# Kernel tuning notes

Hardware: AMD Instinct MI355X
Metric: run time of the kernel (lower is better)

The kernel has to match this reference:

```python
import jax, jax.numpy as jnp
import numpy as np

TRNA_N, DIS_N = 8000, 6000
D, H, E, B = 128, 256, 320000, 16384
NEG_SLOPE = 0.2  # gat_alpha
TEMP = 0.5


def _gat(src, tgt, s_idx, t_idx, Wsrc, Wtgt, a, n_src):
    # BipartiteGraphAttentionLayer (eval mode, dropout off)
    h_i = src @ Wsrc.T            # [n_src, D]
    h_j = tgt @ Wtgt.T            # [n_tgt, D]
    # cat([h_i[s], h_j[t]]) @ a == (h_i @ a[:D])[s] + (h_j @ a[D:])[t]
    s_i = h_i @ a[:D]             # [n_src]
    s_j = h_j @ a[D:]             # [n_tgt]
    e = jax.nn.leaky_relu(s_i[s_idx] + s_j[t_idx], NEG_SLOPE)
    e = jnp.clip(e, -30.0, 30.0)
    exp_e = jnp.exp(e)
    denom = jax.ops.segment_sum(exp_e, s_idx, num_segments=n_src)
    alpha = exp_e / (denom[s_idx] + 1e-8)
    out = jax.ops.segment_sum(h_j[t_idx] * alpha[:, None], s_idx, num_segments=n_src)
    return jax.nn.elu(out)


def _hg(x, S):
    # HCCF-style parameter-free hypergraph conv: nodes -> hyperedges -> nodes
    return jax.nn.elu(S @ (S.T @ x))


def _info_nce(z1, z2):
    z1 = z1 / (jnp.linalg.norm(z1, axis=1, keepdims=True) + 1e-12)
    z2 = z2 / (jnp.linalg.norm(z2, axis=1, keepdims=True) + 1e-12)
    sim = (z1 @ z2.T) / TEMP      # [N, N]
    logp = jax.nn.log_softmax(sim, axis=1)
    return -jnp.mean(jnp.diagonal(logp))


def setup_inputs():
    key = jax.random.key(0)
    ks = jax.random.split(key, 20)
    xn = lambda k, shp, sc: jax.random.normal(k, shp, dtype=jnp.float32) * sc
    d2 = (2.0 / (2 * D)) ** 0.5
    return dict(
        trna_embed=xn(ks[0], (TRNA_N, D), (2.0 / (TRNA_N + D)) ** 0.5),
        disease_embed=xn(ks[1], (DIS_N, D), (2.0 / (DIS_N + D)) ** 0.5),
        thyper=xn(ks[2], (D, H), (2.0 / (D + H)) ** 0.5),
        dhyper=xn(ks[3], (D, H), (2.0 / (D + H)) ** 0.5),
        gat_t_Wsrc=xn(ks[4], (3, D, D), d2),
        gat_t_Wtgt=xn(ks[5], (3, D, D), d2),
        gat_t_a=xn(ks[6], (3, 2 * D), 1.414 * (2.0 / (2 * D + 1)) ** 0.5),
        gat_d_Wsrc=xn(ks[7], (3, D, D), d2),
        gat_d_Wtgt=xn(ks[8], (3, D, D), d2),
        gat_d_a=xn(ks[9], (3, 2 * D), 1.414 * (2.0 / (2 * D + 1)) ** 0.5),
        mlp_W1=xn(ks[10], (D, 2 * D), (2.0 / (3 * D)) ** 0.5),
        mlp_b1=jnp.zeros((D,), jnp.float32),
        mlp_W2=xn(ks[11], (1, D), (2.0 / (D + 1)) ** 0.5),
        mlp_b2=jnp.zeros((1,), jnp.float32),
        gate_W=xn(ks[12], (1, D), (2.0 / (D + 1)) ** 0.5),
        gate_b=jnp.zeros((1,), jnp.float32),
        src_id=jax.random.randint(ks[13], (E,), 0, TRNA_N),
        tgt_id=jax.random.randint(ks[14], (E,), 0, DIS_N),
        trna_ids=jax.random.randint(ks[15], (B,), 0, TRNA_N),
        disease_ids=jax.random.randint(ks[16], (B,), 0, DIS_N),
    )


def reference(trna_embed, disease_embed, thyper, dhyper,
              gat_t_Wsrc, gat_t_Wtgt, gat_t_a,
              gat_d_Wsrc, gat_d_Wtgt, gat_d_a,
              mlp_W1, mlp_b1, mlp_W2, mlp_b2, gate_W, gate_b,
              src_id, tgt_id, trna_ids, disease_ids):
    # stage 1: simple-graph GAT pass
    sg_t = _gat(trna_embed, disease_embed, src_id, tgt_id,
                gat_t_Wsrc[0], gat_t_Wtgt[0], gat_t_a[0], TRNA_N)
    sg_d = _gat(disease_embed, sg_t, tgt_id, src_id,
                gat_d_Wsrc[0], gat_d_Wtgt[0], gat_d_a[0], DIS_N)
    # hypergraph passes 1-2
    hg_t = _hg(sg_t, sg_t @ thyper)
    hg_d = _hg(sg_d, sg_d @ dhyper)
    hg_t = _hg(hg_t, hg_t @ thyper)
    hg_d = _hg(hg_d, hg_d @ dhyper)
    # GAT layers 2-3 on hypergraph outputs
    sg_t = _gat(hg_t, hg_d, src_id, tgt_id,
                gat_t_Wsrc[1], gat_t_Wtgt[1], gat_t_a[1], TRNA_N)
    sg_d = _gat(hg_d, hg_t, tgt_id, src_id,
                gat_d_Wsrc[1], gat_d_Wtgt[1], gat_d_a[1], DIS_N)
    sg_t = _gat(sg_t, sg_d, src_id, tgt_id,
                gat_t_Wsrc[2], gat_t_Wtgt[2], gat_t_a[2], TRNA_N)
    sg_d = _gat(sg_d, sg_t, tgt_id, src_id,
                gat_d_Wsrc[2], gat_d_Wtgt[2], gat_d_a[2], DIS_N)
    # hypergraph pass 3
    hg_t = _hg(hg_t, hg_t @ thyper)
    hg_d = _hg(hg_d, hg_d @ dhyper)
    final_t = sg_t + hg_t
    final_d = sg_d + hg_d
    sel_t = final_t[trna_ids]
    sel_d = final_d[disease_ids]
    contrast = _info_nce(sg_t, hg_t) + _info_nce(sg_d, hg_d)
    gmf_vec = sel_t * sel_d
    gmf_pred = jnp.sum(gmf_vec, axis=-1)
    mlp_in = jnp.concatenate([sel_t, sel_d], axis=-1)
    h1 = jax.nn.relu(mlp_in @ mlp_W1.T + mlp_b1)
    mlp_pred = (h1 @ mlp_W2.T + mlp_b2)[:, 0]
    gate = jax.nn.sigmoid(gmf_vec @ gate_W.T + gate_b)[:, 0]
    fusion_pred = gate * gmf_pred + (1.0 - gate) * mlp_pred
    return (fusion_pred, sg_t, sg_d, gmf_pred, mlp_pred, contrast)
```

## Files before the change

### kernel.cpp

```cpp
#include <hip/hip_runtime.h>
#include <math.h>

#define N_T 8000
#define N_D 6000
#define N_E 320000
#define N_B 16384
#define NSTRIP 24

typedef __attribute__((ext_vector_type(8))) short s16x8;
typedef __attribute__((ext_vector_type(8))) __bf16 bf16x8;
typedef __attribute__((ext_vector_type(4))) float f32x4;

static __device__ __forceinline__ f32x4 mfma16(s16x8 a, s16x8 b, f32x4 c) {
  return __builtin_amdgcn_mfma_f32_16x16x32_bf16(
      __builtin_bit_cast(bf16x8, a), __builtin_bit_cast(bf16x8, b), c, 0, 0, 0);
}

static __device__ __forceinline__ unsigned short f2bf(float f) {
  unsigned u = __float_as_uint(f);
  u += 0x7FFF + ((u >> 16) & 1);
  return (unsigned short)(u >> 16);
}

static __device__ __forceinline__ float bf2f(unsigned short u) {
  return __uint_as_float(((unsigned)u) << 16);
}

__device__ __forceinline__ float wave_sum(float v) {
  v += __shfl_xor(v, 32, 64);
  v += __shfl_xor(v, 16, 64);
  v += __shfl_xor(v, 8, 64);
  v += __shfl_xor(v, 4, 64);
  v += __shfl_xor(v, 2, 64);
  v += __shfl_xor(v, 1, 64);
  return v;
}

__global__ void k_hist2(const int* __restrict__ src, const int* __restrict__ tgt,
                        int* __restrict__ cnt) {
  int i = blockIdx.x * 256 + threadIdx.x;
  if (i < N_E) atomicAdd(&cnt[src[i]], 1);
  else if (i < 2 * N_E) atomicAdd(&cnt[N_T + tgt[i - N_E]], 1);
}

__global__ void k_scan2(const int* __restrict__ cnt, int* __restrict__ rp_t,
    int* __restrict__ cur_t, int* __restrict__ rp_d, int* __restrict__ cur_d) {
  const int* c = blockIdx.x ? cnt + N_T : cnt;
  const int n = blockIdx.x ? N_D : N_T;
  int* rp = blockIdx.x ? rp_d : rp_t;
  int* cur = blockIdx.x ? cur_d : cur_t;
  __shared__ int buf[1024];
  __shared__ int carry_s;
  if (threadIdx.x == 0) carry_s = 0;
  __syncthreads();
  for (int base = 0; base < n; base += 1024) {
    int c0 = carry_s;
    int i = base + (int)threadIdx.x;
    int v = (i < n) ? c[i] : 0;
    buf[threadIdx.x] = v;
    __syncthreads();
    for (int off = 1; off < 1024; off <<= 1) {
      int t = (threadIdx.x >= (unsigned)off) ? buf[threadIdx.x - off] : 0;
      __syncthreads();
      buf[threadIdx.x] += t;
      __syncthreads();
    }
    int incl = buf[threadIdx.x];
    if (i < n) { int e = c0 + incl - v; rp[i] = e; cur[i] = e; }
    __syncthreads();
    if (threadIdx.x == 0) carry_s = c0 + buf[1023];
    __syncthreads();
  }
  if (threadIdx.x == 0) rp[n] = carry_s;
}

__global__ void k_scatter2(const int* __restrict__ src, const int* __restrict__ tgt,
    int* __restrict__ cur_t, int* __restrict__ cur_d,
    int* __restrict__ nbr_t, int* __restrict__ nbr_d) {
  int i = blockIdx.x * 256 + threadIdx.x;
  if (i < N_E) {
    int p = atomicAdd(&cur_t[src[i]], 1);
    nbr_t[p] = tgt[i];
  } else if (i < 2 * N_E) {
    i -= N_E;
    int p = atomicAdd(&cur_d[tgt[i]], 1);
    nbr_d[p] = src[i];
  }
}

__global__ __launch_bounds__(256) void k_pgemm(const float* __restrict__ th,
    const float* __restrict__ dh, float* __restrict__ P_t, float* __restrict__ P_d) {
  const float* A = blockIdx.x < 4 ? th : dh;
  float* C = blockIdx.x < 4 ? P_t : P_d;
  const int sub = blockIdx.x & 3;
  const int row0 = (sub >> 1) * 64, col0 = (sub & 1) * 64;
  __shared__ float As[16][65];
  __shared__ float Bs[16][65];
  const int tid = threadIdx.x;
  const int tr = tid >> 4, tc = tid & 15;
  float acc[4][4] = {};
  for (int k0 = 0; k0 < 256; k0 += 16) {
    {
      int m = tid >> 2, kk = (tid & 3) * 4;
      float4 v = *(const float4*)(A + (size_t)(row0 + m) * 256 + k0 + kk);
      As[kk + 0][m] = v.x; As[kk + 1][m] = v.y; As[kk + 2][m] = v.z; As[kk + 3][m] = v.w;
    }
    {
      int nn = tid >> 2, kk = (tid & 3) * 4;
      float4 v = *(const float4*)(A + (size_t)(col0 + nn) * 256 + k0 + kk);
      Bs[kk + 0][nn] = v.x; Bs[kk + 1][nn] = v.y; Bs[kk + 2][nn] = v.z; Bs[kk + 3][nn] = v.w;
    }
    __syncthreads();
#pragma unroll
    for (int k = 0; k < 16; ++k) {
      float a[4], b[4];
#pragma unroll
      for (int i = 0; i < 4; ++i) a[i] = As[k][tr * 4 + i];
#pragma unroll
      for (int j = 0; j < 4; ++j) b[j] = Bs[k][tc * 4 + j];
#pragma unroll
      for (int i = 0; i < 4; ++i)
#pragma unroll
        for (int j = 0; j < 4; ++j)
          acc[i][j] = fmaf(a[i], b[j], acc[i][j]);
    }
    __syncthreads();
  }
#pragma unroll
  for (int i = 0; i < 4; ++i)
#pragma unroll
    for (int j = 0; j < 4; ++j)
      C[(size_t)(row0 + tr * 4 + i) * 128 + col0 + tc * 4 + j] = acc[i][j];
}

__global__ void k_tobf16m(const float* __restrict__ a0, unsigned short* __restrict__ y0,
    const float* __restrict__ a1, unsigned short* __restrict__ y1,
    const float* __restrict__ a2, unsigned short* __restrict__ y2,
    const float* __restrict__ a3, unsigned short* __restrict__ y3) {
  int i = blockIdx.x * 256 + threadIdx.x;
  const float* x; unsigned short* y;
  if (i < 12288) { x = a0; y = y0; }
  else if (i < 24576) { x = a1; y = y1; i -= 12288; }
  else if (i < 32768) { x = a2; y = y2; i -= 24576; }
  else if (i < 224768) { x = a3; y = y3; i -= 32768; }
  else return;
  float4 v = ((const float4*)x)[i];
  ushort4 o;
  o.x = f2bf(v.x); o.y = f2bf(v.y); o.z = f2bf(v.z); o.w = f2bf(v.w);
  ((ushort4*)y)[i] = o;
}

template<int K, int ACT, int BIAS, int SJMODE, int OUTF, int OUTB>
static __device__ __forceinline__ void mfma_body(
    const unsigned short* __restrict__ A, const unsigned short* __restrict__ B,
    const float* __restrict__ bias, const float* __restrict__ a2,
    float* __restrict__ Cf, unsigned short* __restrict__ Cb,
    float* __restrict__ sj_out, int M, int bx) {
  const int wave = threadIdx.x >> 6, lane = threadIdx.x & 63;
  const int row0 = bx * 32;
  const int col0 = wave * 32;
  const int l15 = lane & 15, kg = lane >> 4;
  constexpr int NS = K / 32;
  f32x4 acc[2][2] = {};
  s16x8 ab[2][2], bb[2][2];
  auto ld = [&](int buf, int k0) {
#pragma unroll
    for (int i = 0; i < 2; ++i) {
      int r = row0 + i * 16 + l15;
      ab[buf][i] = (r < M) ? *(const s16x8*)(A + (size_t)r * K + k0 + kg * 8) : (s16x8)0;
    }
#pragma unroll
    for (int j = 0; j < 2; ++j) {
      int c = col0 + j * 16 + l15;
      bb[buf][j] = *(const s16x8*)(B + (size_t)c * K + k0 + kg * 8);
    }
  };
  ld(0, 0);
#pragma unroll
  for (int s = 0; s < NS; ++s) {
    if (s + 1 < NS) ld((s + 1) & 1, (s + 1) * 32);
#pragma unroll
    for (int i = 0; i < 2; ++i)
#pragma unroll
      for (int j = 0; j < 2; ++j)
        acc[i][j] = mfma16(ab[s & 1][i], bb[s & 1][j], acc[i][j]);
  }
  __shared__ float sjl[4][32];
  float a2v[2];
  if (SJMODE) {
#pragma unroll
    for (int j = 0; j < 2; ++j) a2v[j] = a2[col0 + j * 16 + l15];
  }
#pragma unroll
  for (int i = 0; i < 2; ++i) {
    float part[4] = {0.f, 0.f, 0.f, 0.f};
#pragma unroll
    for (int j = 0; j < 2; ++j) {
      int gc = col0 + j * 16 + l15;
      float bv = BIAS ? bias[gc] : 0.f;
#pragma unroll
      for (int r = 0; r < 4; ++r) {
        int gr = row0 + i * 16 + kg * 4 + r;
        float v = acc[i][j][r] + bv;
        if (SJMODE == 1) part[r] += v * a2v[j];
        if (ACT == 1) v = v > 0.f ? v : __expf(v) - 1.f;
        if (ACT == 2) v = fmaxf(v, 0.f);
        if (SJMODE == 2) part[r] += v * a2v[j];
        if (gr < M) {
          if (OUTF) Cf[(size_t)gr * 128 + gc] = v;
          if (OUTB) Cb[(size_t)gr * 128 + gc] = f2bf(v);
        }
      }
    }
    if (SJMODE) {
#pragma unroll
      for (int r = 0; r < 4; ++r) {
        float p = part[r];
        p += __shfl_xor(p, 1, 64);
        p += __shfl_xor(p, 2, 64);
        p += __shfl_xor(p, 4, 64);
        p += __shfl_xor(p, 8, 64);
        if (l15 == 0) sjl[wave][i * 16 + kg * 4 + r] = p;
      }
    }
  }
  if (SJMODE) {
    __syncthreads();
    if (threadIdx.x < 32) {
      int gr = row0 + (int)threadIdx.x;
      if (gr < M)
        sj_out[gr] = sjl[0][threadIdx.x] + sjl[1][threadIdx.x] +
                     sjl[2][threadIdx.x] + sjl[3][threadIdx.x];
    }
  }
}

template<int K, int ACT, int BIAS, int SJMODE, int OUTF, int OUTB>
__global__ __launch_bounds__(256) void k_mfma(const unsigned short* __restrict__ A,
    const unsigned short* __restrict__ B, const float* __restrict__ bias,
    const float* __restrict__ a2, float* __restrict__ Cf, unsigned short* __restrict__ Cb,
    float* __restrict__ sj_out, int M) {
  mfma_body<K, ACT, BIAS, SJMODE, OUTF, OUTB>(A, B, bias, a2, Cf, Cb, sj_out, M, blockIdx.x);
}

template<int K, int ACT, int SJMODE, int OUTF, int OUTB>
__global__ __launch_bounds__(256) void k_mfma2(
    const unsigned short* __restrict__ A0, const unsigned short* __restrict__ B0,
    const float* __restrict__ a20, float* __restrict__ Cf0,
    unsigned short* __restrict__ Cb0, float* __restrict__ sj0, int M0, int G0,
    const unsigned short* __restrict__ A1, const unsigned short* __restrict__ B1,
    const float* __restrict__ a21, float* __restrict__ Cf1,
    unsigned short* __restrict__ Cb1, float* __restrict__ sj1, int M1) {
  int bx = blockIdx.x;
  if (bx < G0)
    mfma_body<K, ACT, 0, SJMODE, OUTF, OUTB>(A0, B0, nullptr, a20, Cf0, Cb0, sj0, M0, bx);
  else
    mfma_body<K, ACT, 0, SJMODE, OUTF, OUTB>(A1, B1, nullptr, a21, Cf1, Cb1, sj1, M1, bx - G0);
}

__global__ __launch_bounds__(256) void k_nce2m(
    const unsigned short* __restrict__ z1t, const unsigned short* __restrict__ z2t,
    float* __restrict__ rs_tp, float* __restrict__ dg_tp,
    const unsigned short* __restrict__ z1d, const unsigned short* __restrict__ z2d,
    float* __restrict__ rs_dp, float* __restrict__ dg_dp) {
  const int wave = threadIdx.x >> 6, lane = threadIdx.x & 63;
  const int l15 = lane & 15, kg = lane >> 4;
  int by = blockIdx.y;
  const unsigned short *z1, *z2; float *rowsum, *diagv; int M, N;
  if (by < 63) { z1 = z1t; z2 = z2t; rowsum = rs_tp; diagv = dg_tp; M = N_T; N = N_T; }
  else { by -= 63; z1 = z1d; z2 = z2d; rowsum = rs_dp; diagv = dg_dp; M = N_D; N = N_D; }
  const int row0 = by * 128 + (wave >> 1) * 64;
  const int CT = (N + 127) >> 7;
  const int ctps = (CT + NSTRIP - 1) / NSTRIP;
  const int ct0 = blockIdx.x * ctps;
  const int ct1 = min(CT, ct0 + ctps);
  if (ct0 >= CT) return;
  s16x8 a[4][4];
#pragma unroll
  for (int ks = 0; ks < 4; ++ks)
#pragma unroll
    for (int i = 0; i < 4; ++i) {
      int r = row0 + i * 16 + l15;
      a[ks][i] = (r < M) ? *(const s16x8*)(z1 + (size_t)r * 128 + ks * 32 + kg * 8) : (s16x8)0;
    }
  s16x8 b[2][4];
  auto ldb = [&](int buf, int ct, int ks) {
    int c0 = ct * 128 + (wave & 1) * 64;
#pragma unroll
    for (int j = 0; j < 4; ++j) {
      int c = c0 + j * 16 + l15;
      b[buf][j] = (c < N) ? *(const s16x8*)(z2 + (size_t)c * 128 + ks * 32 + kg * 8) : (s16x8)0;
    }
  };
  float rs[4][4] = {};
  ldb(0, ct0, 0);
  for (int ct = ct0; ct < ct1; ++ct) {
    const int col0 = ct * 128 + (wave & 1) * 64;
    f32x4 acc[4][4] = {};
#pragma unroll
    for (int ks = 0; ks < 4; ++ks) {
      if (ks < 3) ldb((ks + 1) & 1, ct, ks + 1);
      else if (ct + 1 < ct1) ldb(0, ct + 1, 0);
#pragma unroll
      for (int i = 0; i < 4; ++i)
#pragma unroll
        for (int j = 0; j < 4; ++j)
          acc[i][j] = mfma16(a[ks][i], b[ks & 1][j], acc[i][j]);
    }
#pragma unroll
    for (int j = 0; j < 4; ++j) {
      int gc = col0 + j * 16 + l15;
      bool cok = gc < N;
#pragma unroll
      for (int i = 0; i < 4; ++i)
#pragma unroll
        for (int r = 0; r < 4; ++r) {
          float sim = acc[i][j][r] * 2.0f;
          if (cok) rs[i][r] += __expf(sim);
          int gr = row0 + i * 16 + kg * 4 + r;
          if (gr == gc && gr < M) diagv[gr] = sim;
        }
    }
  }
#pragma unroll
  for (int i = 0; i < 4; ++i)
#pragma unroll
    for (int r = 0; r < 4; ++r) {
      float v = rs[i][r];
      v += __shfl_xor(v, 1, 64);
      v += __shfl_xor(v, 2, 64);
      v += __shfl_xor(v, 4, 64);
      v += __shfl_xor(v, 8, 64);
      if (l15 == 0) {
        int gr = row0 + i * 16 + kg * 4 + r;
        if (gr < M) atomicAdd(&rowsum[gr], v);
      }
    }
}

__global__ __launch_bounds__(256) void k_syrk2m(const unsigned short* __restrict__ xbT,
    const unsigned short* __restrict__ xbD, float* __restrict__ partT,
    float* __restrict__ partD) {
  int b = blockIdx.x;
  const unsigned short* xb; float* part; int n;
  if (b < 128) { xb = xbT; part = partT + (size_t)b * 16384; n = N_T; }
  else { b -= 128; xb = xbD; part = partD + (size_t)b * 16384; n = N_D; }
  __shared__ float rows[4][128];
  int chunk = (n + 127) >> 7;
  int m0 = b * chunk, m1 = min(n, m0 + chunk);
  int tx = threadIdx.x & 15, ty = threadIdx.x >> 4;
  float acc[8][8] = {};
  for (int m = m0; m < m1; m += 4) {
    int nr = min(4, m1 - m);
    if ((int)threadIdx.x < nr * 64) {
      ushort2 u = ((const ushort2*)(xb + (size_t)m * 128))[threadIdx.x];
      rows[threadIdx.x >> 6][(threadIdx.x & 63) * 2] = bf2f(u.x);
      rows[threadIdx.x >> 6][(threadIdx.x & 63) * 2 + 1] = bf2f(u.y);
    }
    __syncthreads();
    for (int r = 0; r < nr; ++r) {
      float a[8], bv[8];
#pragma unroll
      for (int i = 0; i < 8; ++i) a[i] = rows[r][i * 16 + ty];
#pragma unroll
      for (int j = 0; j < 8; ++j) bv[j] = rows[r][j * 16 + tx];
#pragma unroll
      for (int i = 0; i < 8; ++i)
#pragma unroll
        for (int j = 0; j < 8; ++j)
          acc[i][j] = fmaf(a[i], bv[j], acc[i][j]);
    }
    __syncthreads();
  }
#pragma unroll
  for (int i = 0; i < 8; ++i)
#pragma unroll
    for (int j = 0; j < 8; ++j)
      part[(i * 16 + ty) * 128 + j * 16 + tx] = acc[i][j];
}

__global__ void k_redm(const float* __restrict__ partT, const float* __restrict__ partD,
                       float* __restrict__ GmT, float* __restrict__ GmD) {
  int b = blockIdx.x;
  const float* part = b < 64 ? partT : partD;
  float* G = b < 64 ? GmT : GmD;
  int i = (b & 63) * 256 + threadIdx.x;
  float s = 0.f;
  for (int c = 0; c < 128; ++c) s += part[(size_t)c * 16384 + i];
  G[i] = s;
}

__global__ __launch_bounds__(256) void k_wtm(const float* __restrict__ GmT,
    const float* __restrict__ P_t, unsigned short* __restrict__ wb_t,
    const float* __restrict__ GmD, const float* __restrict__ P_d,
    unsigned short* __restrict__ wb_d) {
  const float* G = blockIdx.x < 4 ? GmT : GmD;
  const float* P = blockIdx.x < 4 ? P_t : P_d;
  unsigned short* wb = blockIdx.x < 4 ? wb_t : wb_d;
  const int sub = blockIdx.x & 3;
  const int bi = sub >> 1, bj = sub & 1;
  __shared__ float Gs[64][129];
  __shared__ float Ps[128][65];
  for (int t = threadIdx.x; t < 8192; t += 256) {
    int il = t >> 7, k = t & 127;
    Gs[il][k] = G[(bi * 64 + il) * 128 + k];
    int pk = t >> 6, pj = t & 63;
    Ps[pk][pj] = P[pk * 128 + bj * 64 + pj];
  }
  __syncthreads();
  const int tx = threadIdx.x & 15, ty = threadIdx.x >> 4;
  float acc[4][4] = {};
  for (int k = 0; k < 128; ++k) {
    float a[4], b[4];
#pragma unroll
    for (int i = 0; i < 4; ++i) a[i] = Gs[ty * 4 + i][k];
#pragma unroll
    for (int j = 0; j < 4; ++j) b[j] = Ps[k][tx * 4 + j];
#pragma unroll
    for (int i = 0; i < 4; ++i)
#pragma unroll
      for (int j = 0; j < 4; ++j)
        acc[i][j] = fmaf(a[i], b[j], acc[i][j]);
  }
#pragma unroll
  for (int i = 0; i < 4; ++i)
#pragma unroll
    for (int j = 0; j < 4; ++j)
      wb[(bi * 64 + ty * 4 + i) * 128 + bj * 64 + tx * 4 + j] = f2bf(acc[i][j]);
}

__global__ void k_wvec6(const float* __restrict__ WsT, const float* __restrict__ aT,
                        const float* __restrict__ WsD, const float* __restrict__ aD,
                        float* __restrict__ wv) {
  int b = blockIdx.x, k = threadIdx.x;
  const float* W = b < 3 ? WsT + b * 16384 : WsD + (b - 3) * 16384;
  const float* a = b < 3 ? aT + b * 256 : aD + (b - 3) * 256;
  float s = 0.f;
  for (int n = 0; n < 128; ++n) s = fmaf(W[n * 128 + k], a[n], s);
  wv[b * 128 + k] = s;
}

__global__ void k_rowdot2(const float* __restrict__ trna, const float* __restrict__ dis,
    const float* __restrict__ wv, float* __restrict__ si_ta, float* __restrict__ si_da) {
  int r = blockIdx.x * 4 + (threadIdx.x >> 6);
  int lane = threadIdx.x & 63;
  const float* h; const float* a; float* o; int row;
  if (r < N_T) { h = trna; a = wv; o = si_ta; row = r; }
  else {
    row = r - N_T;
    if (row >= N_D) return;
    h = dis; a = wv + 3 * 128; o = si_da;
  }
  float2 v = *(const float2*)(h + (size_t)row * 128 + lane * 2);
  float2 av = *(const float2*)(a + lane * 2);
  float s = v.x * av.x + v.y * av.y;
  s = wave_sum(s);
  if (lane == 0) o[row] = s;
}

template<int OUTF, int OUTB, int EMIT_SI>
static __device__ __forceinline__ void agg_body(const int* __restrict__ rp,
    const int* __restrict__ nbr, const float* __restrict__ si,
    const float* __restrict__ sj, const unsigned short* __restrict__ hjb,
    float* __restrict__ outF, unsigned short* __restrict__ outB,
    const float* __restrict__ wv, float* __restrict__ si_out, int n, int bx) {
  int r = bx * 4 + (threadIdx.x >> 6);
  int lane = threadIdx.x & 63;
  if (r >= n) return;
  int p0 = rp[r], p1 = rp[r + 1];
  float sir = si[r];
  int c2 = lane * 2;
  auto wcalc = [&](int t) {
    float v = sir + sj[t];
    v = v >= 0.f ? v : 0.2f * v;
    v = fminf(30.f, fmaxf(-30.f, v));
    return __expf(v);
  };
  float ax = 0.f, ay = 0.f, den = 0.f;
  int p = p0;
  for (; p + 4 <= p1; p += 4) {
    int t0 = nbr[p], t1 = nbr[p + 1], t2 = nbr[p + 2], t3 = nbr[p + 3];
    float w0 = wcalc(t0), w1 = wcalc(t1), w2 = wcalc(t2), w3 = wcalc(t3);
    ushort2 h0 = *(const ushort2*)(hjb + (size_t)t0 * 128 + c2);
    ushort2 h1 = *(const ushort2*)(hjb + (size_t)t1 * 128 + c2);
    ushort2 h2 = *(const ushort2*)(hjb + (size_t)t2 * 128 + c2);
    ushort2 h3 = *(const ushort2*)(hjb + (size_t)t3 * 128 + c2);
    den += (w0 + w1) + (w2 + w3);
    ax += w0 * bf2f(h0.x) + w1 * bf2f(h1.x) + w2 * bf2f(h2.x) + w3 * bf2f(h3.x);
    ay += w0 * bf2f(h0.y) + w1 * bf2f(h1.y) + w2 * bf2f(h2.y) + w3 * bf2f(h3.y);
  }
  for (; p < p1; ++p) {
    int t = nbr[p];
    float w = wcalc(t);
    ushort2 h = *(const ushort2*)(hjb + (size_t)t * 128 + c2);
    den += w;
    ax += w * bf2f(h.x);
    ay += w * bf2f(h.y);
  }
  float inv = 1.0f / (den + 1e-8f);
  float vx = ax * inv, vy = ay * inv;
  vx = vx > 0.f ? vx : __expf(vx) - 1.f;
  vy = vy > 0.f ? vy : __expf(vy) - 1.f;
  if (OUTF) {
    float2 of; of.x = vx; of.y = vy;
    *(float2*)(outF + (size_t)r * 128 + c2) = of;
  }
  if (OUTB) {
    ushort2 ob; ob.x = f2bf(vx); ob.y = f2bf(vy);
    *(ushort2*)(outB + (size_t)r * 128 + c2) = ob;
  }
  if (EMIT_SI) {
    float2 w2v = *(const float2*)(wv + c2);
    float d = vx * w2v.x + vy * w2v.y;
    d = wave_sum(d);
    if (lane == 0) si_out[r] = d;
  }
}

template<int OUTF, int OUTB, int EMIT_SI>
__global__ __launch_bounds__(256) void k_agg(const int* __restrict__ rp,
    const int* __restrict__ nbr, const float* __restrict__ si,
    const float* __restrict__ sj, const unsigned short* __restrict__ hjb,
    float* __restrict__ outF, unsigned short* __restrict__ outB,
    const float* __restrict__ wv, float* __restrict__ si_out, int n) {
  agg_body<OUTF, OUTB, EMIT_SI>(rp, nbr, si, sj, hjb, outF, outB, wv, si_out, n, blockIdx.x);
}

template<int OUTF, int OUTB, int EMIT_SI>
__global__ __launch_bounds__(256) void k_agg2(
    const int* __restrict__ rp0, const int* __restrict__ nbr0, const float* __restrict__ si0,
    const float* __restrict__ sj0, const unsigned short* __restrict__ hjb0,
    float* __restrict__ outF0, unsigned short* __restrict__ outB0,
    const float* __restrict__ wv0, float* __restrict__ sio0, int n0, int G0,
    const int* __restrict__ rp1, const int* __restrict__ nbr1, const float* __restrict__ si1,
    const float* __restrict__ sj1, const unsigned short* __restrict__ hjb1,
    float* __restrict__ outF1, unsigned short* __restrict__ outB1,
    const float* __restrict__ wv1, float* __restrict__ sio1, int n1) {
  int bx = blockIdx.x;
  if (bx < G0)
    agg_body<OUTF, OUTB, EMIT_SI>(rp0, nbr0, si0, sj0, hjb0, outF0, outB0, wv0, sio0, n0, bx);
  else
    agg_body<OUTF, OUTB, EMIT_SI>(rp1, nbr1, si1, sj1, hjb1, outF1, outB1, wv1, sio1, n1, bx - G0);
}

__global__ void k_norm4(const float* __restrict__ sgt, const float* __restrict__ hgt3,
    const float* __restrict__ sgd, const float* __restrict__ hgd3,
    unsigned short* __restrict__ z1t, unsigned short* __restrict__ z2t,
    unsigned short* __restrict__ z1d, unsigned short* __restrict__ z2d,
    float* __restrict__ rs_t, float* __restrict__ rs_d) {
  int ridx = blockIdx.x * 4 + (threadIdx.x >> 6);
  int lane = threadIdx.x & 63;
  const float* src; unsigned short* dst; int row; float* rsz = nullptr;
  if (ridx < 8000)       { src = sgt;  dst = z1t; row = ridx;         rsz = rs_t; }
  else if (ridx < 16000) { src = hgt3; dst = z2t; row = ridx - 8000; }
  else if (ridx < 22000) { src = sgd;  dst = z1d; row = ridx - 16000; rsz = rs_d; }
  else if (ridx < 28000) { src = hgd3; dst = z2d; row = ridx - 22000; }
  else return;
  float2 v = *(const float2*)(src + (size_t)row * 128 + lane * 2);
  float ss = v.x * v.x + v.y * v.y;
  ss = wave_sum(ss);
  float inv = 1.0f / (sqrtf(ss) + 1e-12f);
  ushort2 o; o.x = f2bf(v.x * inv); o.y = f2bf(v.y * inv);
  *(ushort2*)(dst + (size_t)row * 128 + lane * 2) = o;
  if (rsz && lane == 0) rsz[row] = 0.f;
}

__global__ void k_gather(const float* __restrict__ sgt, const float* __restrict__ hgt,
    const float* __restrict__ sgd, const float* __restrict__ hgd,
    const int* __restrict__ tids, const int* __restrict__ dids,
    const float* __restrict__ gateW, unsigned short* __restrict__ mlp_in_b,
    float* __restrict__ gmf, float* __restrict__ gate_lin, int nB) {
  int b = blockIdx.x * 4 + (threadIdx.x >> 6);
  int lane = threadIdx.x & 63;
  if (b >= nB) return;
  int ti = tids[b], di = dids[b];
  float2 a1 = *(const float2*)(sgt + (size_t)ti * 128 + lane * 2);
  float2 a2 = *(const float2*)(hgt + (size_t)ti * 128 + lane * 2);
  float2 c1 = *(const float2*)(sgd + (size_t)di * 128 + lane * 2);
  float2 c2 = *(const float2*)(hgd + (size_t)di * 128 + lane * 2);
  float2 st; st.x = a1.x + a2.x; st.y = a1.y + a2.y;
  float2 sd; sd.x = c1.x + c2.x; sd.y = c1.y + c2.y;
  ushort2 o1; o1.x = f2bf(st.x); o1.y = f2bf(st.y);
  ushort2 o2; o2.x = f2bf(sd.x); o2.y = f2bf(sd.y);
  *(ushort2*)(mlp_in_b + (size_t)b * 256 + lane * 2) = o1;
  *(ushort2*)(mlp_in_b + (size_t)b * 256 + 128 + lane * 2) = o2;
  float2 gv; gv.x = st.x * sd.x; gv.y = st.y * sd.y;
  float2 gw = *(const float2*)(gateW + lane * 2);
  float s1 = gv.x + gv.y;
  float s2 = gv.x * gw.x + gv.y * gw.y;
  s1 = wave_sum(s1);
  s2 = wave_sum(s2);
  if (lane == 0) { gmf[b] = s1; gate_lin[b] = s2; }
}

__global__ void k_final(const float* __restrict__ h1, const float* __restrict__ W2,
    const float* __restrict__ b2, const float* __restrict__ gate_lin,
    const float* __restrict__ gate_b, const float* __restrict__ gmf,
    float* __restrict__ fusion, float* __restrict__ mlp_pred, int nB) {
  int b = blockIdx.x * 4 + (threadIdx.x >> 6);
  int lane = threadIdx.x & 63;
  if (b >= nB) return;
  float2 hv = *(const float2*)(h1 + (size_t)b * 128 + lane * 2);
  float2 wv = *(const float2*)(W2 + lane * 2);
  float s = hv.x * wv.x + hv.y * wv.y;
  s = wave_sum(s);
  if (lane == 0) {
    float mp = s + b2[0];
    float g = 1.0f / (1.0f + __expf(-(gate_lin[b] + gate_b[0])));
    mlp_pred[b] = mp;
    fusion[b] = g * gmf[b] + (1.0f - g) * mp;
  }
}

__global__ void k_contrast(const float* __restrict__ rs_t, const float* __restrict__ dg_t,
    const float* __restrict__ rs_d, const float* __restrict__ dg_d, float* __restrict__ out) {
  __shared__ float red[256];
  float st = 0.f, sd = 0.f;
  for (int i = threadIdx.x; i < N_T; i += 256) st += __logf(rs_t[i]) - dg_t[i];
  for (int i = threadIdx.x; i < N_D; i += 256) sd += __logf(rs_d[i]) - dg_d[i];
  red[threadIdx.x] = st * (1.0f / N_T) + sd * (1.0f / N_D);
  __syncthreads();
  for (int off = 128; off; off >>= 1) {
    if (threadIdx.x < (unsigned)off) red[threadIdx.x] += red[threadIdx.x + off];
    __syncthreads();
  }
  if (threadIdx.x == 0) out[0] = red[0];
}

extern "C" void kernel_launch(void* const* d_in, const int* in_sizes, int n_in,
                              void* d_out, int out_size, void* d_ws, size_t ws_size,
                              hipStream_t stream) {
  const float* trna   = (const float*)d_in[0];
  const float* dis    = (const float*)d_in[1];
  const float* thyper = (const float*)d_in[2];
  const float* dhyper = (const float*)d_in[3];
  const float* WsrcT  = (const float*)d_in[4];
  const float* WtgtT  = (const float*)d_in[5];
  const float* aT     = (const float*)d_in[6];
  const float* WsrcD  = (const float*)d_in[7];
  const float* WtgtD  = (const float*)d_in[8];
  const float* aD     = (const float*)d_in[9];
  const float* W1     = (const float*)d_in[10];
  const float* b1     = (const float*)d_in[11];
  const float* W2     = (const float*)d_in[12];
  const float* b2     = (const float*)d_in[13];
  const float* gW     = (const float*)d_in[14];
  const float* gb     = (const float*)d_in[15];
  const int* src_id   = (const int*)d_in[16];
  const int* tgt_id   = (const int*)d_in[17];
  const int* tids     = (const int*)d_in[18];
  const int* dids     = (const int*)d_in[19];
  float* out = (float*)d_out;

  float* out_fusion = out;
  float* out_sgt    = out + 16384;
  float* out_sgd    = out + 16384 + 1024000;
  float* out_gmf    = out + 1808384;
  float* out_mlp    = out + 1824768;
  float* out_con    = out + 1841152;

  char* wsb = (char*)d_ws;
  size_t off = 0;
  auto alloc = [&](size_t bytes) -> void* {
    void* p = wsb + off;
    off += (bytes + 255) & ~(size_t)255;
    return p;
  };
  float* hg_t3  = (float*)alloc((size_t)N_T * 128 * 4);
  float* hg_d3  = (float*)alloc((size_t)N_D * 128 * 4);
  unsigned short* sgt_b  = (unsigned short*)alloc((size_t)N_T * 128 * 2);
  unsigned short* sgd_b  = (unsigned short*)alloc((size_t)N_D * 128 * 2);
  unsigned short* hgt_b  = (unsigned short*)alloc((size_t)N_T * 128 * 2);
  unsigned short* hgd_b  = (unsigned short*)alloc((size_t)N_D * 128 * 2);
  unsigned short* hgt2_b = (unsigned short*)alloc((size_t)N_T * 128 * 2);
  unsigned short* hgd2_b = (unsigned short*)alloc((size_t)N_D * 128 * 2);
  unsigned short* disb   = (unsigned short*)alloc((size_t)N_D * 128 * 2);
  unsigned short* hjbT   = (unsigned short*)alloc((size_t)N_T * 128 * 2);
  unsigned short* hjbD   = (unsigned short*)alloc((size_t)N_T * 128 * 2);
  unsigned short* zb1t = (unsigned short*)alloc((size_t)N_T * 128 * 2);
  unsigned short* zb2t = (unsigned short*)alloc((size_t)N_T * 128 * 2);
  unsigned short* zb1d = (unsigned short*)alloc((size_t)N_D * 128 * 2);
  unsigned short* zb2d = (unsigned short*)alloc((size_t)N_D * 128 * 2);
  unsigned short* wb_t = (unsigned short*)alloc(16384 * 2);
  unsigned short* wb_d = (unsigned short*)alloc(16384 * 2);
  unsigned short* wbT  = (unsigned short*)alloc(3 * 16384 * 2);
  unsigned short* wbD  = (unsigned short*)alloc(3 * 16384 * 2);
  unsigned short* W1b  = (unsigned short*)alloc(32768 * 2);
  unsigned short* mlp_in_b = (unsigned short*)alloc((size_t)N_B * 256 * 2);
  float* h1buf  = (float*)alloc((size_t)N_B * 128 * 4);
  float* partT  = (float*)mlp_in_b;
  float* partD  = partT + (size_t)128 * 16384;
  float* Gm_t   = (float*)alloc(16384 * 4);
  float* Gm_d   = (float*)alloc(16384 * 4);
  float* P_t    = (float*)alloc(16384 * 4);
  float* P_d    = (float*)alloc(16384 * 4);
  float* wvecs  = (float*)alloc(6 * 128 * 4);
  float* si_ta  = (float*)alloc(N_T * 4);
  float* si_tb  = (float*)alloc(N_T * 4);
  float* si_da  = (float*)alloc(N_D * 4);
  float* si_db  = (float*)alloc(N_D * 4);
  float* s_jT   = (float*)alloc(N_T * 4);
  float* s_jD   = (float*)alloc(N_T * 4);
  int* cnt      = (int*)alloc((N_T + N_D) * 4);
  int* rp_t     = (int*)alloc((N_T + 1) * 4);
  int* cur_t    = (int*)alloc(N_T * 4);
  int* rp_d     = (int*)alloc((N_D + 1) * 4);
  int* cur_d    = (int*)alloc(N_D * 4);
  int* nbrc_t   = (int*)alloc((size_t)N_E * 4);
  int* nbrc_d   = (int*)alloc((size_t)N_E * 4);
  float* rs_t   = (float*)alloc(N_T * 4);
  float* dg_t   = (float*)alloc(N_T * 4);
  float* rs_d   = (float*)alloc(N_D * 4);
  float* dg_d   = (float*)alloc(N_D * 4);
  float* g_lin  = (float*)alloc(N_B * 4);
  (void)ws_size; (void)in_sizes; (void)n_in; (void)out_size;

  const int gT32 = (N_T + 31) / 32;
  const int gD32 = (N_D + 31) / 32;
  const int aT4 = (N_T + 3) / 4, aD4 = (N_D + 3) / 4;

  hipMemsetAsync(cnt, 0, (N_T + N_D) * 4, stream);
  k_hist2<<<(2 * N_E + 255) / 256, 256, 0, stream>>>(src_id, tgt_id, cnt);
  k_scan2<<<2, 1024, 0, stream>>>(cnt, rp_t, cur_t, rp_d, cur_d);
  k_scatter2<<<(2 * N_E + 255) / 256, 256, 0, stream>>>(src_id, tgt_id, cur_t, cur_d,
      nbrc_t, nbrc_d);

  k_pgemm<<<8, 256, 0, stream>>>(thyper, dhyper, P_t, P_d);
  k_wvec6<<<6, 128, 0, stream>>>(WsrcT, aT, WsrcD, aD, wvecs);
  k_tobf16m<<<878, 256, 0, stream>>>(WtgtT, wbT, WtgtD, wbD, W1, W1b, dis, disb);
  k_rowdot2<<<(N_T + N_D + 3) / 4, 256, 0, stream>>>(trna, dis, wvecs, si_ta, si_da);

  k_mfma<128, 0, 0, 1, 0, 1><<<gD32, 256, 0, stream>>>(
      disb, wbT, nullptr, aT + 128, nullptr, hjbT, s_jT, N_D);
  k_agg<0, 1, 0><<<aT4, 256, 0, stream>>>(rp_t, nbrc_t, si_ta, s_jT, hjbT,
      nullptr, sgt_b, nullptr, nullptr, N_T);
  k_mfma<128, 0, 0, 1, 0, 1><<<gT32, 256, 0, stream>>>(
      sgt_b, wbD, nullptr, aD + 128, nullptr, hjbD, s_jD, N_T);
  k_agg<0, 1, 0><<<aD4, 256, 0, stream>>>(rp_d, nbrc_d, si_da, s_jD, hjbD,
      nullptr, sgd_b, nullptr, nullptr, N_D);

  k_syrk2m<<<256, 256, 0, stream>>>(sgt_b, sgd_b, partT, partD);
  k_redm<<<128, 256, 0, stream>>>(partT, partD, Gm_t, Gm_d);
  k_wtm<<<8, 256, 0, stream>>>(Gm_t, P_t, wb_t, Gm_d, P_d, wb_d);
  k_mfma2<128, 1, 0, 0, 1><<<gT32 + gD32, 256, 0, stream>>>(
      sgt_b, wb_t, nullptr, nullptr, hgt_b, nullptr, N_T, gT32,
      sgd_b, wb_d, nullptr, nullptr, hgd_b, nullptr, N_D);

  k_syrk2m<<<256, 256, 0, stream>>>(hgt_b, hgd_b, partT, partD);
  k_redm<<<128, 256, 0, stream>>>(partT, partD, Gm_t, Gm_d);
  k_wtm<<<8, 256, 0, stream>>>(Gm_t, P_t, wb_t, Gm_d, P_d, wb_d);
  k_mfma2<128, 1, 2, 0, 1><<<gT32 + gD32, 256, 0, stream>>>(
      hgt_b, wb_t, wvecs + 128, nullptr, hgt2_b, si_tb, N_T, gT32,
      hgd_b, wb_d, wvecs + 4 * 128, nullptr, hgd2_b, si_db, N_D);

  k_mfma2<128, 0, 1, 0, 1><<<gD32 + gT32, 256, 0, stream>>>(
      hgd2_b, wbT + 16384, aT + 256 + 128, nullptr, hjbT, s_jT, N_D, gD32,
      hgt2_b, wbD + 16384, aD + 256 + 128, nullptr, hjbD, s_jD, N_T);
  k_agg2<0, 1, 1><<<aT4 + aD4, 256, 0, stream>>>(
      rp_t, nbrc_t, si_tb, s_jT, hjbT, nullptr, sgt_b, wvecs + 2 * 128, si_ta, N_T, aT4,
      rp_d, nbrc_d, si_db, s_jD, hjbD, nullptr, sgd_b, wvecs + 5 * 128, si_da, N_D);

  k_mfma<128, 0, 0, 1, 0, 1><<<gD32, 256, 0, stream>>>(
      sgd_b, wbT + 32768, nullptr, aT + 512 + 128, nullptr, hjbT, s_jT, N_D);
  k_agg<1, 1, 0><<<aT4, 256, 0, stream>>>(rp_t, nbrc_t, si_ta, s_jT, hjbT,
      out_sgt, sgt_b, nullptr, nullptr, N_T);
  k_mfma<128, 0, 0, 1, 0, 1><<<gT32, 256, 0, stream>>>(
      sgt_b, wbD + 32768, nullptr, aD + 512 + 128, nullptr, hjbD, s_jD, N_T);
  k_agg<1, 0, 0><<<aD4, 256, 0, stream>>>(rp_d, nbrc_d, si_da, s_jD, hjbD,
      out_sgd, nullptr, nullptr, nullptr, N_D);

  k_syrk2m<<<256, 256, 0, stream>>>(hgt2_b, hgd2_b, partT, partD);
  k_redm<<<128, 256, 0, stream>>>(partT, partD, Gm_t, Gm_d);
  k_wtm<<<8, 256, 0, stream>>>(Gm_t, P_t, wb_t, Gm_d, P_d, wb_d);
  k_mfma2<128, 1, 0, 1, 0><<<gT32 + gD32, 256, 0, stream>>>(
      hgt2_b, wb_t, nullptr, hg_t3, nullptr, nullptr, N_T, gT32,
      hgd2_b, wb_d, nullptr, hg_d3, nullptr, nullptr, N_D);

  k_norm4<<<7000, 256, 0, stream>>>(out_sgt, hg_t3, out_sgd, hg_d3,
      zb1t, zb2t, zb1d, zb2d, rs_t, rs_d);
  k_nce2m<<<dim3(NSTRIP, 63 + 47), 256, 0, stream>>>(
      zb1t, zb2t, rs_t, dg_t, zb1d, zb2d, rs_d, dg_d);
  k_contrast<<<1, 256, 0, stream>>>(rs_t, dg_t, rs_d, dg_d, out_con);

  k_gather<<<(N_B + 3) / 4, 256, 0, stream>>>(out_sgt, hg_t3, out_sgd, hg_d3,
      tids, dids, gW, mlp_in_b, out_gmf, g_lin, N_B);
  k_mfma<256, 2, 1, 0, 1, 0><<<N_B / 32, 256, 0, stream>>>(
      mlp_in_b, W1b, b1, nullptr, h1buf, nullptr, nullptr, N_B);
  k_final<<<(N_B + 3) / 4, 256, 0, stream>>>(h1buf, W2, b2, g_lin, gb,
      out_gmf, out_fusion, out_mlp, N_B);
}
```

Baseline: 509.5 us.

## Stage InfoNCE column tiles in LDS, widen aggregation lanes, fuse norm with diagonal

The InfoNCE similarity kernel now loads each 128-column tile of z2 cooperatively into XOR-swizzled shared memory, so all four waves reuse it instead of each fetching from global. The strip count drops from 24 to 8, giving each block more column tiles. The diagonal logits move into a fused normalization kernel that processes both z1 and z2 rows and computes their dot product. Separately, the GAT aggregation uses 32 lanes per row with 4-element vector loads, so each 256-thread block covers 8 rows. The trade-offs are a barrier per tile, no register prefetch of the next tile, and fewer blocks in the NCE grid.

```diff
diff --git a/kernel.cpp b/kernel.cpp
--- a/kernel.cpp
+++ b/kernel.cpp
@@ -5,7 +5,7 @@
 #define N_D 6000
 #define N_E 320000
 #define N_B 16384
-#define NSTRIP 24
+#define NSTRIP 8
 
 typedef __attribute__((ext_vector_type(8))) short s16x8;
 typedef __attribute__((ext_vector_type(8))) __bf16 bf16x8;
@@ -28,6 +28,15 @@
 
 __device__ __forceinline__ float wave_sum(float v) {
   v += __shfl_xor(v, 32, 64);
+  v += __shfl_xor(v, 16, 64);
+  v += __shfl_xor(v, 8, 64);
+  v += __shfl_xor(v, 4, 64);
+  v += __shfl_xor(v, 2, 64);
+  v += __shfl_xor(v, 1, 64);
+  return v;
+}
+
+__device__ __forceinline__ float half_sum(float v) {
   v += __shfl_xor(v, 16, 64);
   v += __shfl_xor(v, 8, 64);
   v += __shfl_xor(v, 4, 64);
@@ -258,18 +267,20 @@
     mfma_body<K, ACT, 0, SJMODE, OUTF, OUTB>(A1, B1, nullptr, a21, Cf1, Cb1, sj1, M1, bx - G0);
 }
 
-__global__ __launch_bounds__(256) void k_nce2m(
+__global__ __launch_bounds__(256) void k_nce3(
     const unsigned short* __restrict__ z1t, const unsigned short* __restrict__ z2t,
-    float* __restrict__ rs_tp, float* __restrict__ dg_tp,
+    float* __restrict__ rs_tp,
     const unsigned short* __restrict__ z1d, const unsigned short* __restrict__ z2d,
-    float* __restrict__ rs_dp, float* __restrict__ dg_dp) {
+    float* __restrict__ rs_dp) {
+  __shared__ unsigned short bt[128 * 128];
   const int wave = threadIdx.x >> 6, lane = threadIdx.x & 63;
   const int l15 = lane & 15, kg = lane >> 4;
   int by = blockIdx.y;
-  const unsigned short *z1, *z2; float *rowsum, *diagv; int M, N;
-  if (by < 63) { z1 = z1t; z2 = z2t; rowsum = rs_tp; diagv = dg_tp; M = N_T; N = N_T; }
-  else { by -= 63; z1 = z1d; z2 = z2d; rowsum = rs_dp; diagv = dg_dp; M = N_D; N = N_D; }
+  const unsigned short *z1, *z2; float* rowsum; int M, N;
+  if (by < 63) { z1 = z1t; z2 = z2t; rowsum = rs_tp; M = N_T; N = N_T; }
+  else { by -= 63; z1 = z1d; z2 = z2d; rowsum = rs_dp; M = N_D; N = N_D; }
   const int row0 = by * 128 + (wave >> 1) * 64;
+  const int colw = (wave & 1) * 64;
   const int CT = (N + 127) >> 7;
   const int ctps = (CT + NSTRIP - 1) / NSTRIP;
   const int ct0 = blockIdx.x * ctps;
@@ -283,44 +294,46 @@
       int r = row0 + i * 16 + l15;
       a[ks][i] = (r < M) ? *(const s16x8*)(z1 + (size_t)r * 128 + ks * 32 + kg * 8) : (s16x8)0;
     }
-  s16x8 b[2][4];
-  auto ldb = [&](int buf, int ct, int ks) {
-    int c0 = ct * 128 + (wave & 1) * 64;
+  float rs[4][4] = {};
+  for (int ct = ct0; ct < ct1; ++ct) {
+    const int cbase = ct * 128;
+#pragma unroll
+    for (int i = 0; i < 8; ++i) {
+      int c = i * 256 + (int)threadIdx.x;
+      int trow = c >> 4, ks = c & 15;
+      int rg = cbase + trow;
+      rg = rg < N ? rg : N - 1;
+      s16x8 v = *(const s16x8*)(z2 + (size_t)rg * 128 + ks * 8);
+      *(s16x8*)((char*)bt + trow * 256 + ((ks * 16) ^ ((trow & 7) << 4))) = v;
+    }
+    __syncthreads();
+    f32x4 acc[4][4] = {};
+#pragma unroll
+    for (int ks = 0; ks < 4; ++ks) {
+      s16x8 b[4];
+#pragma unroll
+      for (int j = 0; j < 4; ++j) {
+        int trow = colw + j * 16 + l15;
+        b[j] = *(const s16x8*)((const char*)bt + trow * 256 +
+                               ((ks * 64 + kg * 16) ^ ((trow & 7) << 4)));
+      }
+#pragma unroll
+      for (int i = 0; i < 4; ++i)
+#pragma unroll
+        for (int j = 0; j < 4; ++j)
+          acc[i][j] = mfma16(a[ks][i], b[j], acc[i][j]);
+    }
 #pragma unroll
     for (int j = 0; j < 4; ++j) {
-      int c = c0 + j * 16 + l15;
-      b[buf][j] = (c < N) ? *(const s16x8*)(z2 + (size_t)c * 128 + ks * 32 + kg * 8) : (s16x8)0;
-    }
-  };
-  float rs[4][4] = {};
-  ldb(0, ct0, 0);
-  for (int ct = ct0; ct < ct1; ++ct) {
-    const int col0 = ct * 128 + (wave & 1) * 64;
-    f32x4 acc[4][4] = {};
-#pragma unroll
-    for (int ks = 0; ks < 4; ++ks) {
-      if (ks < 3) ldb((ks + 1) & 1, ct, ks + 1);
-      else if (ct + 1 < ct1) ldb(0, ct + 1, 0);
+      int gc = cbase + colw + j * 16 + l15;
+      bool cok = gc < N;
 #pragma unroll
       for (int i = 0; i < 4; ++i)
 #pragma unroll
-        for (int j = 0; j < 4; ++j)
-          acc[i][j] = mfma16(a[ks][i], b[ks & 1][j], acc[i][j]);
-    }
-#pragma unroll
-    for (int j = 0; j < 4; ++j) {
-      int gc = col0 + j * 16 + l15;
-      bool cok = gc < N;
-#pragma unroll
-      for (int i = 0; i < 4; ++i)
-#pragma unroll
-        for (int r = 0; r < 4; ++r) {
-          float sim = acc[i][j][r] * 2.0f;
-          if (cok) rs[i][r] += __expf(sim);
-          int gr = row0 + i * 16 + kg * 4 + r;
-          if (gr == gc && gr < M) diagv[gr] = sim;
-        }
-    }
+        for (int r = 0; r < 4; ++r)
+          if (cok) rs[i][r] += __expf(acc[i][j][r] * 2.0f);
+    }
+    __syncthreads();
   }
 #pragma unroll
   for (int i = 0; i < 4; ++i)
@@ -464,55 +477,63 @@
     const float* __restrict__ sj, const unsigned short* __restrict__ hjb,
     float* __restrict__ outF, unsigned short* __restrict__ outB,
     const float* __restrict__ wv, float* __restrict__ si_out, int n, int bx) {
-  int r = bx * 4 + (threadIdx.x >> 6);
-  int lane = threadIdx.x & 63;
+  int r = bx * 8 + ((int)threadIdx.x >> 5);
+  int lane = threadIdx.x & 31;
   if (r >= n) return;
   int p0 = rp[r], p1 = rp[r + 1];
   float sir = si[r];
-  int c2 = lane * 2;
+  int c4 = lane * 4;
   auto wcalc = [&](int t) {
     float v = sir + sj[t];
     v = v >= 0.f ? v : 0.2f * v;
     v = fminf(30.f, fmaxf(-30.f, v));
     return __expf(v);
   };
-  float ax = 0.f, ay = 0.f, den = 0.f;
+  float a0 = 0.f, a1 = 0.f, a2 = 0.f, a3 = 0.f, den = 0.f;
   int p = p0;
   for (; p + 4 <= p1; p += 4) {
     int t0 = nbr[p], t1 = nbr[p + 1], t2 = nbr[p + 2], t3 = nbr[p + 3];
     float w0 = wcalc(t0), w1 = wcalc(t1), w2 = wcalc(t2), w3 = wcalc(t3);
-    ushort2 h0 = *(const ushort2*)(hjb + (size_t)t0 * 128 + c2);
-    ushort2 h1 = *(const ushort2*)(hjb + (size_t)t1 * 128 + c2);
-    ushort2 h2 = *(const ushort2*)(hjb + (size_t)t2 * 128 + c2);
-    ushort2 h3 = *(const ushort2*)(hjb + (size_t)t3 * 128 + c2);
+    ushort4 h0 = *(const ushort4*)(hjb + (size_t)t0 * 128 + c4);
+    ushort4 h1 = *(const ushort4*)(hjb + (size_t)t1 * 128 + c4);
+    ushort4 h2 = *(const ushort4*)(hjb + (size_t)t2 * 128 + c4);
+    ushort4 h3 = *(const ushort4*)(hjb + (size_t)t3 * 128 + c4);
     den += (w0 + w1) + (w2 + w3);
-    ax += w0 * bf2f(h0.x) + w1 * bf2f(h1.x) + w2 * bf2f(h2.x) + w3 * bf2f(h3.x);
-    ay += w0 * bf2f(h0.y) + w1 * bf2f(h1.y) + w2 * bf2f(h2.y) + w3 * bf2f(h3.y);
+    a0 += w0 * bf2f(h0.x) + w1 * bf2f(h1.x) + w2 * bf2f(h2.x) + w3 * bf2f(h3.x);
+    a1 += w0 * bf2f(h0.y) + w1 * bf2f(h1.y) + w2 * bf2f(h2.y) + w3 * bf2f(h3.y);
+    a2 += w0 * bf2f(h0.z) + w1 * bf2f(h1.z) + w2 * bf2f(h2.z) + w3 * bf2f(h3.z);
+    a3 += w0 * bf2f(h0.w) + w1 * bf2f(h1.w) + w2 * bf2f(h2.w) + w3 * bf2f(h3.w);
   }
   for (; p < p1; ++p) {
     int t = nbr[p];
     float w = wcalc(t);
-    ushort2 h = *(const ushort2*)(hjb + (size_t)t * 128 + c2);
+    ushort4 h = *(const ushort4*)(hjb + (size_t)t * 128 + c4);
     den += w;
-    ax += w * bf2f(h.x);
-    ay += w * bf2f(h.y);
+    a0 += w * bf2f(h.x); a1 += w * bf2f(h.y);
+    a2 += w * bf2f(h.z); a3 += w * bf2f(h.w);
   }
   float inv = 1.0f / (den + 1e-8f);
-  float vx = ax * inv, vy = ay * inv;
-  vx = vx > 0.f ? vx : __expf(vx) - 1.f;
-  vy = vy > 0.f ? vy : __expf(vy) - 1.f;
+  float v0 = a0 * inv, v1 = a1 * inv, v2 = a2 * inv, v3 = a3 * inv;
+  v0 = v0 > 0.f ? v0 : __expf(v0) - 1.f;
+  v1 = v1 > 0.f ? v1 : __expf(v1) - 1.f;
+  v2 = v2 > 0.f ? v2 : __expf(v2) - 1.f;
+  v3 = v3 > 0.f ? v3 : __expf(v3) - 1.f;
   if (OUTF) {
-    float2 of; of.x = vx; of.y = vy;
-    *(float2*)(outF + (size_t)r * 128 + c2) = of;
+    float4 of; of.x = v0; of.y = v1; of.z = v2; of.w = v3;
+    *(float4*)(outF + (size_t)r * 128 + c4) = of;
   }
   if (OUTB) {
-    ushort2 ob; ob.x = f2bf(vx); ob.y = f2bf(vy);
-    *(ushort2*)(outB + (size_t)r * 128 + c2) = ob;
+    ushort4 ob; ob.x = f2bf(v0); ob.y = f2bf(v1); ob.z = f2bf(v2); ob.w = f2bf(v3);
+    *(ushort4*)(outB + (size_t)r * 128 + c4) = ob;
   }
   if (EMIT_SI) {
-    float2 w2v = *(const float2*)(wv + c2);
-    float d = vx * w2v.x + vy * w2v.y;
-    d = wave_sum(d);
+    float4 w4 = *(const float4*)(wv + c4);
+    float d = v0 * w4.x + v1 * w4.y + v2 * w4.z + v3 * w4.w;
+    d += __shfl_xor(d, 16, 64);
+    d += __shfl_xor(d, 8, 64);
+    d += __shfl_xor(d, 4, 64);
+    d += __shfl_xor(d, 2, 64);
+    d += __shfl_xor(d, 1, 64);
     if (lane == 0) si_out[r] = d;
   }
 }
@@ -543,26 +564,34 @@
     agg_body<OUTF, OUTB, EMIT_SI>(rp1, nbr1, si1, sj1, hjb1, outF1, outB1, wv1, sio1, n1, bx - G0);
 }
 
-__global__ void k_norm4(const float* __restrict__ sgt, const float* __restrict__ hgt3,
+__global__ void k_norm2(const float* __restrict__ sgt, const float* __restrict__ hgt3,
     const float* __restrict__ sgd, const float* __restrict__ hgd3,
     unsigned short* __restrict__ z1t, unsigned short* __restrict__ z2t,
     unsigned short* __restrict__ z1d, unsigned short* __restrict__ z2d,
-    float* __restrict__ rs_t, float* __restrict__ rs_d) {
+    float* __restrict__ rs_t, float* __restrict__ dg_t,
+    float* __restrict__ rs_d, float* __restrict__ dg_d) {
   int ridx = blockIdx.x * 4 + (threadIdx.x >> 6);
   int lane = threadIdx.x & 63;
-  const float* src; unsigned short* dst; int row; float* rsz = nullptr;
-  if (ridx < 8000)       { src = sgt;  dst = z1t; row = ridx;         rsz = rs_t; }
-  else if (ridx < 16000) { src = hgt3; dst = z2t; row = ridx - 8000; }
-  else if (ridx < 22000) { src = sgd;  dst = z1d; row = ridx - 16000; rsz = rs_d; }
-  else if (ridx < 28000) { src = hgd3; dst = z2d; row = ridx - 22000; }
-  else return;
-  float2 v = *(const float2*)(src + (size_t)row * 128 + lane * 2);
-  float ss = v.x * v.x + v.y * v.y;
-  ss = wave_sum(ss);
-  float inv = 1.0f / (sqrtf(ss) + 1e-12f);
-  ushort2 o; o.x = f2bf(v.x * inv); o.y = f2bf(v.y * inv);
-  *(ushort2*)(dst + (size_t)row * 128 + lane * 2) = o;
-  if (rsz && lane == 0) rsz[row] = 0.f;
+  const float *x1, *x2; unsigned short *o1, *o2; float *rs, *dg; int row;
+  if (ridx < 8000) { x1 = sgt; x2 = hgt3; o1 = z1t; o2 = z2t; rs = rs_t; dg = dg_t; row = ridx; }
+  else if (ridx < 14000) {
+    row = ridx - 8000;
+    x1 = sgd; x2 = hgd3; o1 = z1d; o2 = z2d; rs = rs_d; dg = dg_d;
+  } else return;
+  float2 v1 = *(const float2*)(x1 + (size_t)row * 128 + lane * 2);
+  float2 v2 = *(const float2*)(x2 + (size_t)row * 128 + lane * 2);
+  float ss1 = wave_sum(v1.x * v1.x + v1.y * v1.y);
+  float ss2 = wave_sum(v2.x * v2.x + v2.y * v2.y);
+  float i1 = 1.0f / (sqrtf(ss1) + 1e-12f);
+  float i2 = 1.0f / (sqrtf(ss2) + 1e-12f);
+  float n1x = v1.x * i1, n1y = v1.y * i1;
+  float n2x = v2.x * i2, n2y = v2.y * i2;
+  ushort2 w1; w1.x = f2bf(n1x); w1.y = f2bf(n1y);
+  ushort2 w2; w2.x = f2bf(n2x); w2.y = f2bf(n2y);
+  *(ushort2*)(o1 + (size_t)row * 128 + lane * 2) = w1;
+  *(ushort2*)(o2 + (size_t)row * 128 + lane * 2) = w2;
+  float d = wave_sum(n1x * n2x + n1y * n2y);
+  if (lane == 0) { dg[row] = 2.0f * d; rs[row] = 0.f; }
 }
 
 __global__ void k_gather(const float* __restrict__ sgt, const float* __restrict__ hgt,
@@ -717,7 +746,7 @@
 
   const int gT32 = (N_T + 31) / 32;
   const int gD32 = (N_D + 31) / 32;
-  const int aT4 = (N_T + 3) / 4, aD4 = (N_D + 3) / 4;
+  const int aT8 = (N_T + 7) / 8, aD8 = (N_D + 7) / 8;
 
   hipMemsetAsync(cnt, 0, (N_T + N_D) * 4, stream);
   k_hist2<<<(2 * N_E + 255) / 256, 256, 0, stream>>>(src_id, tgt_id, cnt);
@@ -732,11 +761,11 @@
 
   k_mfma<128, 0, 0, 1, 0, 1><<<gD32, 256, 0, stream>>>(
       disb, wbT, nullptr, aT + 128, nullptr, hjbT, s_jT, N_D);
-  k_agg<0, 1, 0><<<aT4, 256, 0, stream>>>(rp_t, nbrc_t, si_ta, s_jT, hjbT,
+  k_agg<0, 1, 0><<<aT8, 256, 0, stream>>>(rp_t, nbrc_t, si_ta, s_jT, hjbT,
       nullptr, sgt_b, nullptr, nullptr, N_T);
   k_mfma<128, 0, 0, 1, 0, 1><<<gT32, 256, 0, stream>>>(
       sgt_b, wbD, nullptr, aD + 128, nullptr, hjbD, s_jD, N_T);
-  k_agg<0, 1, 0><<<aD4, 256, 0, stream>>>(rp_d, nbrc_d, si_da, s_jD, hjbD,
+  k_agg<0, 1, 0><<<aD8, 256, 0, stream>>>(rp_d, nbrc_d, si_da, s_jD, hjbD,
       nullptr, sgd_b, nullptr, nullptr, N_D);
 
   k_syrk2m<<<256, 256, 0, stream>>>(sgt_b, sgd_b, partT, partD);
@@ -756,17 +785,17 @@
   k_mfma2<128, 0, 1, 0, 1><<<gD32 + gT32, 256, 0, stream>>>(
       hgd2_b, wbT + 16384, aT + 256 + 128, nullptr, hjbT, s_jT, N_D, gD32,
       hgt2_b, wbD + 16384, aD + 256 + 128, nullptr, hjbD, s_jD, N_T);
-  k_agg2<0, 1, 1><<<aT4 + aD4, 256, 0, stream>>>(
-      rp_t, nbrc_t, si_tb, s_jT, hjbT, nullptr, sgt_b, wvecs + 2 * 128, si_ta, N_T, aT4,
+  k_agg2<0, 1, 1><<<aT8 + aD8, 256, 0, stream>>>(
+      rp_t, nbrc_t, si_tb, s_jT, hjbT, nullptr, sgt_b, wvecs + 2 * 128, si_ta, N_T, aT8,
       rp_d, nbrc_d, si_db, s_jD, hjbD, nullptr, sgd_b, wvecs + 5 * 128, si_da, N_D);
 
   k_mfma<128, 0, 0, 1, 0, 1><<<gD32, 256, 0, stream>>>(
       sgd_b, wbT + 32768, nullptr, aT + 512 + 128, nullptr, hjbT, s_jT, N_D);
-  k_agg<1, 1, 0><<<aT4, 256, 0, stream>>>(rp_t, nbrc_t, si_ta, s_jT, hjbT,
+  k_agg<1, 1, 0><<<aT8, 256, 0, stream>>>(rp_t, nbrc_t, si_ta, s_jT, hjbT,
       out_sgt, sgt_b, nullptr, nullptr, N_T);
   k_mfma<128, 0, 0, 1, 0, 1><<<gT32, 256, 0, stream>>>(
       sgt_b, wbD + 32768, nullptr, aD + 512 + 128, nullptr, hjbD, s_jD, N_T);
-  k_agg<1, 0, 0><<<aD4, 256, 0, stream>>>(rp_d, nbrc_d, si_da, s_jD, hjbD,
+  k_agg<1, 0, 0><<<aD8, 256, 0, stream>>>(rp_d, nbrc_d, si_da, s_jD, hjbD,
       out_sgd, nullptr, nullptr, nullptr, N_D);
 
   k_syrk2m<<<256, 256, 0, stream>>>(hgt2_b, hgd2_b, partT, partD);
@@ -776,10 +805,10 @@
       hgt2_b, wb_t, nullptr, hg_t3, nullptr, nullptr, N_T, gT32,
       hgd2_b, wb_d, nullptr, hg_d3, nullptr, nullptr, N_D);
 
-  k_norm4<<<7000, 256, 0, stream>>>(out_sgt, hg_t3, out_sgd, hg_d3,
-      zb1t, zb2t, zb1d, zb2d, rs_t, rs_d);
-  k_nce2m<<<dim3(NSTRIP, 63 + 47), 256, 0, stream>>>(
-      zb1t, zb2t, rs_t, dg_t, zb1d, zb2d, rs_d, dg_d);
+  k_norm2<<<3500, 256, 0, stream>>>(out_sgt, hg_t3, out_sgd, hg_d3,
+      zb1t, zb2t, zb1d, zb2d, rs_t, dg_t, rs_d, dg_d);
+  k_nce3<<<dim3(NSTRIP, 63 + 47), 256, 0, stream>>>(
+      zb1t, zb2t, rs_t, zb1d, zb2d, rs_d);
   k_contrast<<<1, 256, 0, stream>>>(rs_t, dg_t, rs_d, dg_d, out_con);
 
   k_gather<<<(N_B + 3) / 4, 256, 0, stream>>>(out_sgt, hg_t3, out_sgd, hg_d3,
```

New measurement: 488.2 us. -4.2%, faster.
